# Performance work log

Hardware: AMD Instinct MI355X
Metric: run time of the kernel (lower is better)

The kernel has to match this reference:

```python
import jax, jax.numpy as jnp
import numpy as np

WIDTH = 1.0  # radial_width
AMPLITUDE = (WIDTH ** 0.5) * 1.772637204826652  # ~sqrt(pi*width)
BN_EPS = 1e-3  # keras BatchNormalization default


def sine_pos_encoding(seq_len, hidden, dtype):
    # keras_nlp.layers.SinePositionEncoding, max_wavelength=10000
    position = jnp.arange(seq_len, dtype=dtype)
    min_freq = jnp.asarray(1.0 / 10000.0, dtype)
    timescales = min_freq ** (2 * (jnp.arange(hidden) // 2).astype(dtype) / hidden)
    angles = position[:, None] * timescales[None, :]  # [T, H]
    odd = (jnp.arange(hidden) % 2).astype(dtype)
    return jnp.sin(angles) * (1 - odd) + jnp.cos(angles) * odd


def setup_inputs() -> dict:
    key = jax.random.key(0)
    ks = jax.random.split(key, 4)
    B, T, C, F, K, L = 16, 4096, 8, 64, 11, 4096
    x = jax.random.normal(ks[0], (B, T, C), jnp.float32)
    conv_w = jax.random.normal(ks[1], (K, C, F), jnp.float32) * 0.1
    conv_b = jnp.zeros((F,), jnp.float32)
    gamma = jnp.ones((F,), jnp.float32)
    beta = jnp.zeros((F,), jnp.float32)
    mean = jnp.zeros((F,), jnp.float32)
    var = jnp.ones((F,), jnp.float32)
    # HeNormal init for dense
    dense_w = jax.random.normal(ks[2], (F, L), jnp.float32) * (2.0 / F) ** 0.5
    dense_b = jnp.zeros((L,), jnp.float32)
    return dict(x=x, conv_w=conv_w, conv_b=conv_b, gamma=gamma, beta=beta,
                mean=mean, var=var, dense_w=dense_w, dense_b=dense_b)


def reference(x, conv_w, conv_b, gamma, beta, mean, var, dense_w, dense_b):
    B, T, C = x.shape
    F = conv_w.shape[-1]
    L = dense_w.shape[-1]
    # Conv1D same padding -> [B, T, F]
    h = jax.lax.conv_general_dilated(x, conv_w, (1,), 'SAME',
                                     dimension_numbers=('NWC', 'WIO', 'NWC')) + conv_b
    # BatchNorm (inference form)
    h = (h - mean) / jnp.sqrt(var + BN_EPS) * gamma + beta
    # Softmax over time axis
    h = jax.nn.softmax(h, axis=1)
    # sine positional encoding added
    h = h + sine_pos_encoding(T, F, x.dtype)
    # Dense with sigmoid, rescale to [-1, 1]
    d = jax.nn.sigmoid(h @ dense_w + dense_b) * 2.0 - 1.0  # [B, T, L]
    # ReductionLayer: sum over time -> shift weights [B, L]
    shift = jnp.sum(d, axis=1)
    # ShiftingLayer: Gaussian RBF warp matrix then matmul
    idx_in = jnp.arange(1, T + 1, dtype=x.dtype)                       # [T]
    scale = jnp.asarray(T / L, x.dtype)
    idx_sh = (jnp.arange(1, L + 1, dtype=x.dtype) + shift) * scale     # [B, L]
    M = idx_in[None, None, :] - idx_sh[:, :, None]                     # [B, L, T]
    M = jnp.exp(-(M * M) / WIDTH) / AMPLITUDE
    return jnp.matmul(M, x)  # [B, L, C]
```

## Files before the change

### kernel.cpp

```cpp
#include <hip/hip_runtime.h>
#include <stdint.h>

#define BB 16
#define TT 4096
#define CC 8
#define FF 64
#define KW 11
#define LL 4096

typedef __attribute__((ext_vector_type(8))) short short8;
typedef __attribute__((ext_vector_type(16))) float floatx16;

__device__ __forceinline__ unsigned short f2b(float f) {
    union { float f; uint32_t i; } v; v.f = f;
    uint32_t x = v.i;
    return (unsigned short)((x + 0x7fffu + ((x >> 16) & 1u)) >> 16);
}
__device__ __forceinline__ float b2f(unsigned short u) {
    union { uint32_t i; float f; } v; v.i = ((uint32_t)u) << 16; return v.f;
}

__global__ __launch_bounds__(256) void k_split(
        const float* __restrict__ dw, unsigned short* __restrict__ Wt) {
    const int idx  = blockIdx.x * 256 + threadIdx.x;
    const int j    = idx & 7;
    const int ln   = (idx >> 3) & 31;
    const int half = (idx >> 8) & 1;
    const int kf   = (idx >> 9) & 3;
    const int lt   = idx >> 11;
    const int l = lt * 32 + ln;
    const int k = kf * 16 + half * 8 + j;
    const float v = dw[(size_t)k * LL + l];
    const unsigned short hi = f2b(v);
    const unsigned short lo = f2b(v - b2f(hi));
    Wt[idx] = hi;
    Wt[262144 + idx] = lo;
}

__global__ __launch_bounds__(256) void k_sumexp(
        const float* __restrict__ x, const float* __restrict__ cw,
        const float* __restrict__ cb, const float* __restrict__ gm,
        const float* __restrict__ bt, const float* __restrict__ mn,
        const float* __restrict__ vr, float* __restrict__ sumexp) {
    __shared__ __align__(16) float xsm[(64 + KW - 1) * CC];
    __shared__ float red[4 * FF];
    const int tid = threadIdx.x;
    const int b  = blockIdx.x / (TT / 64);
    const int t0 = (blockIdx.x % (TT / 64)) * 64;
    const int f = tid & 63, ts = tid >> 6;

    float wreg[KW * CC];
#pragma unroll
    for (int kc = 0; kc < KW * CC; ++kc) wreg[kc] = cw[kc * FF + f];

    for (int i = tid; i < (64 + KW - 1) * CC; i += 256) {
        int row = i >> 3, c = i & 7;
        int t = t0 - (KW / 2) + row;
        xsm[i] = (t >= 0 && t < TT) ? x[((size_t)b * TT + t) * CC + c] : 0.0f;
    }
    const float s  = gm[f] * rsqrtf(vr[f] + 1e-3f);
    const float bb = bt[f] + (cb[f] - mn[f]) * s;
    __syncthreads();

    const float4* xv = (const float4*)xsm;
    float esum = 0.f;
#pragma unroll 2
    for (int i = 0; i < 16; ++i) {
        const int tt = ts + 4 * i;
        float acc = 0.f;
#pragma unroll
        for (int k = 0; k < KW; ++k) {
            const float4 xa = xv[(tt + k) * 2];
            const float4 xb = xv[(tt + k) * 2 + 1];
            acc = fmaf(xa.x, wreg[k * 8 + 0], acc);
            acc = fmaf(xa.y, wreg[k * 8 + 1], acc);
            acc = fmaf(xa.z, wreg[k * 8 + 2], acc);
            acc = fmaf(xa.w, wreg[k * 8 + 3], acc);
            acc = fmaf(xb.x, wreg[k * 8 + 4], acc);
            acc = fmaf(xb.y, wreg[k * 8 + 5], acc);
            acc = fmaf(xb.z, wreg[k * 8 + 6], acc);
            acc = fmaf(xb.w, wreg[k * 8 + 7], acc);
        }
        esum += __expf(fmaf(acc, s, bb));
    }
    red[ts * FF + f] = esum;
    __syncthreads();
    if (ts == 0) {
        float tot = red[f] + red[FF + f] + red[2 * FF + f] + red[3 * FF + f];
        atomicAdd(&sumexp[b * FF + f], tot);
    }
}

__global__ __launch_bounds__(256) void k_main(
        const float* __restrict__ x,  const float* __restrict__ cw,
        const float* __restrict__ cb, const float* __restrict__ gm,
        const float* __restrict__ bt, const float* __restrict__ mn,
        const float* __restrict__ vr, const unsigned short* __restrict__ Wt,
        const float* __restrict__ db, const float* __restrict__ sumexp,
        float* __restrict__ shiftsum) {
    __shared__ __align__(16) unsigned short As[16384];
    __shared__ __align__(16) float xsm[(128 + KW - 1) * CC];

    const int tid = threadIdx.x;
    const int b  = blockIdx.y;
    const int t0 = blockIdx.x * 128;
    const int f = tid & 63, tq = tid >> 6;

    float wreg[KW * CC];
#pragma unroll
    for (int kc = 0; kc < KW * CC; ++kc) wreg[kc] = cw[kc * FF + f];

    for (int i = tid; i < (128 + KW - 1) * CC; i += 256) {
        int row = i >> 3, c = i & 7;
        int t = t0 - (KW / 2) + row;
        xsm[i] = (t >= 0 && t < TT) ? x[((size_t)b * TT + t) * CC + c] : 0.0f;
    }
    const float s   = gm[f] * rsqrtf(vr[f] + 1e-3f);
    const float bbv = bt[f] + (cb[f] - mn[f]) * s;
    const float inv_se = 1.0f / sumexp[b * FF + f];
    const float tsf = exp2f(-0.20762050586796017f * (float)(f & ~1));
    const int kfh = ((f >> 4) << 1) | ((f >> 3) & 1);
    const int jj  = f & 7;
    __syncthreads();

    const float4* xv = (const float4*)xsm;
#pragma unroll 2
    for (int i = 0; i < 32; ++i) {
        const int tt = tq + 4 * i;
        float acc = 0.f;
#pragma unroll
        for (int k = 0; k < KW; ++k) {
            const float4 xa = xv[(tt + k) * 2];
            const float4 xb = xv[(tt + k) * 2 + 1];
            acc = fmaf(xa.x, wreg[k * 8 + 0], acc);
            acc = fmaf(xa.y, wreg[k * 8 + 1], acc);
            acc = fmaf(xa.z, wreg[k * 8 + 2], acc);
            acc = fmaf(xa.w, wreg[k * 8 + 3], acc);
            acc = fmaf(xb.x, wreg[k * 8 + 4], acc);
            acc = fmaf(xb.y, wreg[k * 8 + 5], acc);
            acc = fmaf(xb.z, wreg[k * 8 + 6], acc);
            acc = fmaf(xb.w, wreg[k * 8 + 7], acc);
        }
        float e = __expf(fmaf(acc, s, bbv));
        float ang = (float)(t0 + tt) * tsf;
        float p = (f & 1) ? cosf(ang) : sinf(ang);
        float h = fmaf(e, inv_se, p);
        const unsigned short hi = f2b(h);
        const unsigned short lo = f2b(h - b2f(hi));
        const int off = ((tt >> 5) * 8 + kfh) * 256 + (tt & 31) * 8 + jj;
        As[off] = hi;
        As[8192 + off] = lo;
    }
    __syncthreads();

    const int lane = tid & 63;
    const int wv   = tid >> 6;
    const int half = lane >> 5;
    const int ln31 = lane & 31;
    const int vbase = (half << 9) | (ln31 << 4);
    const char* Ab = (const char*)As;
    const char* Wb = (const char*)Wt;

    short8 Ahi[16], Alo[16];
#pragma unroll
    for (int nt = 0; nt < 4; ++nt)
#pragma unroll
        for (int kf = 0; kf < 4; ++kf) {
            const int ao = (nt * 8 + kf * 2) << 9;
            Ahi[nt * 4 + kf] = *reinterpret_cast<const short8*>(Ab + ao + vbase);
            Alo[nt * 4 + kf] = *reinterpret_cast<const short8*>(Ab + 16384 + ao + vbase);
        }

#pragma unroll 1
    for (int lt = 0; lt < 32; ++lt) {
        const int ltile = lt * 4 + wv;
        const int lbase = ltile * 32;
        const char* wp = Wb + ((size_t)ltile << 12) + vbase;
        short8 Whi[4], Wlo[4];
#pragma unroll
        for (int kf = 0; kf < 4; ++kf) {
            Whi[kf] = *reinterpret_cast<const short8*>(wp + kf * 1024);
            Wlo[kf] = *reinterpret_cast<const short8*>(wp + 524288 + kf * 1024);
        }
        const float dbl = db[lbase + ln31];

        float ss[4] = {0.f, 0.f, 0.f, 0.f};
#pragma unroll
        for (int nt = 0; nt < 4; ++nt) {
            floatx16 acc = {0.f, 0.f, 0.f, 0.f, 0.f, 0.f, 0.f, 0.f,
                            0.f, 0.f, 0.f, 0.f, 0.f, 0.f, 0.f, 0.f};
#pragma unroll
            for (int kf = 0; kf < 4; ++kf) {
                acc = __builtin_amdgcn_mfma_f32_32x32x16_bf16(Ahi[nt * 4 + kf], Whi[kf], acc, 0, 0, 0);
                acc = __builtin_amdgcn_mfma_f32_32x32x16_bf16(Alo[nt * 4 + kf], Whi[kf], acc, 0, 0, 0);
                acc = __builtin_amdgcn_mfma_f32_32x32x16_bf16(Ahi[nt * 4 + kf], Wlo[kf], acc, 0, 0, 0);
            }
#pragma unroll
            for (int r = 0; r < 16; ++r) {
                float z = acc[r] + dbl;
                float e = __expf(-z);
                ss[r & 3] += __builtin_amdgcn_rcpf(1.0f + e);
            }
        }
        float ssum = (ss[0] + ss[1]) + (ss[2] + ss[3]);
        ssum += __shfl_xor(ssum, 32);
        if (half == 0)
            atomicAdd(shiftsum + (size_t)b * LL + lbase + ln31, ssum);
    }
}

__global__ __launch_bounds__(256) void k_warp(
        const float* __restrict__ shiftsum, const float* __restrict__ x,
        float* __restrict__ out) {
    const int idx = blockIdx.x * 256 + threadIdx.x;
    const int l = idx & (LL - 1);
    const int b = idx >> 12;
    const float sh = fmaf(2.0f, shiftsum[idx], -(float)TT);
    const float scale = (float)TT / (float)LL;
    const float center = ((float)(l + 1) + sh) * scale;
    const float R = 7.0f;
    int tlo = (int)ceilf(center - 1.0f - R);
    int thi = (int)floorf(center - 1.0f + R);
    if (tlo < 0) tlo = 0;
    if (thi > TT - 1) thi = TT - 1;
    float acc[CC];
#pragma unroll
    for (int c = 0; c < CC; ++c) acc[c] = 0.f;
    const float inv_amp = (float)(1.0 / 1.772637204826652);
    for (int t = tlo; t <= thi; ++t) {
        float d = (float)(t + 1) - center;
        float w = __expf(-d * d) * inv_amp;
        const float4 x0 = *reinterpret_cast<const float4*>(x + ((size_t)b * TT + t) * CC);
        const float4 x1 = *reinterpret_cast<const float4*>(x + ((size_t)b * TT + t) * CC + 4);
        acc[0] = fmaf(w, x0.x, acc[0]);
        acc[1] = fmaf(w, x0.y, acc[1]);
        acc[2] = fmaf(w, x0.z, acc[2]);
        acc[3] = fmaf(w, x0.w, acc[3]);
        acc[4] = fmaf(w, x1.x, acc[4]);
        acc[5] = fmaf(w, x1.y, acc[5]);
        acc[6] = fmaf(w, x1.z, acc[6]);
        acc[7] = fmaf(w, x1.w, acc[7]);
    }
    float* o = out + (size_t)idx * CC;
    *reinterpret_cast<float4*>(o)     = make_float4(acc[0], acc[1], acc[2], acc[3]);
    *reinterpret_cast<float4*>(o + 4) = make_float4(acc[4], acc[5], acc[6], acc[7]);
}

extern "C" void kernel_launch(void* const* d_in, const int* in_sizes, int n_in,
                              void* d_out, int out_size, void* d_ws, size_t ws_size,
                              hipStream_t stream) {
    const float* x  = (const float*)d_in[0];
    const float* cw = (const float*)d_in[1];
    const float* cb = (const float*)d_in[2];
    const float* gm = (const float*)d_in[3];
    const float* bt = (const float*)d_in[4];
    const float* mn = (const float*)d_in[5];
    const float* vr = (const float*)d_in[6];
    const float* dw = (const float*)d_in[7];
    const float* db = (const float*)d_in[8];

    float* sumexp      = (float*)d_ws;
    float* shiftsum    = sumexp + BB * FF;
    unsigned short* Wt = (unsigned short*)(shiftsum + BB * LL);

    hipMemsetAsync(sumexp, 0, (size_t)(BB * FF + BB * LL) * sizeof(float), stream);

    k_split<<<(FF * LL) / 256, 256, 0, stream>>>(dw, Wt);
    k_sumexp<<<BB * (TT / 64), 256, 0, stream>>>(x, cw, cb, gm, bt, mn, vr, sumexp);
    k_main<<<dim3(TT / 128, BB), 256, 0, stream>>>(x, cw, cb, gm, bt, mn, vr,
                                                   Wt, db, sumexp, shiftsum);
    k_warp<<<(BB * LL) / 256, 256, 0, stream>>>(shiftsum, x, (float*)d_out);
}
```

Before: 219.9 us.

## Raise k_main to 512 threads, stream A from LDS, cheapen exp/sin/sigmoid math

k_main now runs 8 waves per block. Each wave handles half as many conv rows and L-tiles as before. A-fragments are reloaded from LDS inside the MFMA loop instead of being kept in 32 registers, which cuts register pressure so the tighter launch bounds can allow more resident waves. Per-row sin/cos calls are replaced by a rotation recurrence, and __expf is replaced by exp2 with pre-scaled constants. In the sigmoid reduction, four reciprocals are merged into one. Risks: 512,4 launch bounds may force spills of the 88-float conv weights, and the merged reciprocal can overflow for large exponents.

```diff
diff --git a/kernel.cpp b/kernel.cpp
--- a/kernel.cpp
+++ b/kernel.cpp
@@ -7,6 +7,8 @@
 #define FF 64
 #define KW 11
 #define LL 4096
+
+#define L2E 1.442695040888963f
 
 typedef __attribute__((ext_vector_type(8))) short short8;
 typedef __attribute__((ext_vector_type(16))) float floatx16;
@@ -60,6 +62,7 @@
     }
     const float s  = gm[f] * rsqrtf(vr[f] + 1e-3f);
     const float bb = bt[f] + (cb[f] - mn[f]) * s;
+    const float s2 = s * L2E, b2 = bb * L2E;
     __syncthreads();
 
     const float4* xv = (const float4*)xsm;
@@ -81,7 +84,7 @@
             acc = fmaf(xb.z, wreg[k * 8 + 6], acc);
             acc = fmaf(xb.w, wreg[k * 8 + 7], acc);
         }
-        esum += __expf(fmaf(acc, s, bb));
+        esum += __builtin_amdgcn_exp2f(fmaf(acc, s2, b2));
     }
     red[ts * FF + f] = esum;
     __syncthreads();
@@ -91,7 +94,7 @@
     }
 }
 
-__global__ __launch_bounds__(256) void k_main(
+__global__ __launch_bounds__(512, 4) void k_main(
         const float* __restrict__ x,  const float* __restrict__ cw,
         const float* __restrict__ cb, const float* __restrict__ gm,
         const float* __restrict__ bt, const float* __restrict__ mn,
@@ -110,23 +113,28 @@
 #pragma unroll
     for (int kc = 0; kc < KW * CC; ++kc) wreg[kc] = cw[kc * FF + f];
 
-    for (int i = tid; i < (128 + KW - 1) * CC; i += 256) {
+    for (int i = tid; i < (128 + KW - 1) * CC; i += 512) {
         int row = i >> 3, c = i & 7;
         int t = t0 - (KW / 2) + row;
         xsm[i] = (t >= 0 && t < TT) ? x[((size_t)b * TT + t) * CC + c] : 0.0f;
     }
     const float s   = gm[f] * rsqrtf(vr[f] + 1e-3f);
     const float bbv = bt[f] + (cb[f] - mn[f]) * s;
+    const float s2 = s * L2E, b2 = bbv * L2E;
     const float inv_se = 1.0f / sumexp[b * FF + f];
     const float tsf = exp2f(-0.20762050586796017f * (float)(f & ~1));
     const int kfh = ((f >> 4) << 1) | ((f >> 3) & 1);
     const int jj  = f & 7;
+    const float ang0 = (float)(t0 + tq) * tsf;
+    const float dA = 8.0f * tsf;
+    float sv = sinf(ang0), cv = cosf(ang0);
+    const float sd = sinf(dA), cd = cosf(dA);
     __syncthreads();
 
     const float4* xv = (const float4*)xsm;
 #pragma unroll 2
-    for (int i = 0; i < 32; ++i) {
-        const int tt = tq + 4 * i;
+    for (int i = 0; i < 16; ++i) {
+        const int tt = tq + 8 * i;
         float acc = 0.f;
 #pragma unroll
         for (int k = 0; k < KW; ++k) {
@@ -141,15 +149,17 @@
             acc = fmaf(xb.z, wreg[k * 8 + 6], acc);
             acc = fmaf(xb.w, wreg[k * 8 + 7], acc);
         }
-        float e = __expf(fmaf(acc, s, bbv));
-        float ang = (float)(t0 + tt) * tsf;
-        float p = (f & 1) ? cosf(ang) : sinf(ang);
+        float e = __builtin_amdgcn_exp2f(fmaf(acc, s2, b2));
+        float p = (f & 1) ? cv : sv;
         float h = fmaf(e, inv_se, p);
         const unsigned short hi = f2b(h);
         const unsigned short lo = f2b(h - b2f(hi));
         const int off = ((tt >> 5) * 8 + kfh) * 256 + (tt & 31) * 8 + jj;
         As[off] = hi;
         As[8192 + off] = lo;
+        float ns = fmaf(sv, cd, cv * sd);
+        float nc = fmaf(cv, cd, -(sv * sd));
+        sv = ns; cv = nc;
     }
     __syncthreads();
 
@@ -161,19 +171,9 @@
     const char* Ab = (const char*)As;
     const char* Wb = (const char*)Wt;
 
-    short8 Ahi[16], Alo[16];
-#pragma unroll
-    for (int nt = 0; nt < 4; ++nt)
-#pragma unroll
-        for (int kf = 0; kf < 4; ++kf) {
-            const int ao = (nt * 8 + kf * 2) << 9;
-            Ahi[nt * 4 + kf] = *reinterpret_cast<const short8*>(Ab + ao + vbase);
-            Alo[nt * 4 + kf] = *reinterpret_cast<const short8*>(Ab + 16384 + ao + vbase);
-        }
-
 #pragma unroll 1
-    for (int lt = 0; lt < 32; ++lt) {
-        const int ltile = lt * 4 + wv;
+    for (int lt = 0; lt < 16; ++lt) {
+        const int ltile = lt * 8 + wv;
         const int lbase = ltile * 32;
         const char* wp = Wb + ((size_t)ltile << 12) + vbase;
         short8 Whi[4], Wlo[4];
@@ -182,7 +182,7 @@
             Whi[kf] = *reinterpret_cast<const short8*>(wp + kf * 1024);
             Wlo[kf] = *reinterpret_cast<const short8*>(wp + 524288 + kf * 1024);
         }
-        const float dbl = db[lbase + ln31];
+        const float dbn = db[lbase + ln31] * (-L2E);
 
         float ss[4] = {0.f, 0.f, 0.f, 0.f};
 #pragma unroll
@@ -191,15 +191,23 @@
                             0.f, 0.f, 0.f, 0.f, 0.f, 0.f, 0.f, 0.f};
 #pragma unroll
             for (int kf = 0; kf < 4; ++kf) {
-                acc = __builtin_amdgcn_mfma_f32_32x32x16_bf16(Ahi[nt * 4 + kf], Whi[kf], acc, 0, 0, 0);
-                acc = __builtin_amdgcn_mfma_f32_32x32x16_bf16(Alo[nt * 4 + kf], Whi[kf], acc, 0, 0, 0);
-                acc = __builtin_amdgcn_mfma_f32_32x32x16_bf16(Ahi[nt * 4 + kf], Wlo[kf], acc, 0, 0, 0);
+                const int ao = (nt * 8 + kf * 2) << 9;
+                short8 Ahi = *reinterpret_cast<const short8*>(Ab + ao + vbase);
+                short8 Alo = *reinterpret_cast<const short8*>(Ab + 16384 + ao + vbase);
+                acc = __builtin_amdgcn_mfma_f32_32x32x16_bf16(Ahi, Whi[kf], acc, 0, 0, 0);
+                acc = __builtin_amdgcn_mfma_f32_32x32x16_bf16(Alo, Whi[kf], acc, 0, 0, 0);
+                acc = __builtin_amdgcn_mfma_f32_32x32x16_bf16(Ahi, Wlo[kf], acc, 0, 0, 0);
             }
 #pragma unroll
-            for (int r = 0; r < 16; ++r) {
-                float z = acc[r] + dbl;
-                float e = __expf(-z);
-                ss[r & 3] += __builtin_amdgcn_rcpf(1.0f + e);
+            for (int q = 0; q < 4; ++q) {
+                float e0 = __builtin_amdgcn_exp2f(fmaf(acc[4 * q + 0], -L2E, dbn));
+                float e1 = __builtin_amdgcn_exp2f(fmaf(acc[4 * q + 1], -L2E, dbn));
+                float e2 = __builtin_amdgcn_exp2f(fmaf(acc[4 * q + 2], -L2E, dbn));
+                float e3 = __builtin_amdgcn_exp2f(fmaf(acc[4 * q + 3], -L2E, dbn));
+                float a0 = 1.f + e0, a1 = 1.f + e1, a2 = 1.f + e2, a3 = 1.f + e3;
+                float p01 = a0 * a1, p23 = a2 * a3;
+                float num = fmaf(a0 + a1, p23, (a2 + a3) * p01);
+                ss[q] = fmaf(num, __builtin_amdgcn_rcpf(p01 * p23), ss[q]);
             }
         }
         float ssum = (ss[0] + ss[1]) + (ss[2] + ss[3]);
@@ -267,7 +275,7 @@
 
     k_split<<<(FF * LL) / 256, 256, 0, stream>>>(dw, Wt);
     k_sumexp<<<BB * (TT / 64), 256, 0, stream>>>(x, cw, cb, gm, bt, mn, vr, sumexp);
-    k_main<<<dim3(TT / 128, BB), 256, 0, stream>>>(x, cw, cb, gm, bt, mn, vr,
+    k_main<<<dim3(TT / 128, BB), 512, 0, stream>>>(x, cw, cb, gm, bt, mn, vr,
                                                    Wt, db, sumexp, shiftsum);
     k_warp<<<(BB * LL) / 256, 256, 0, stream>>>(shiftsum, x, (float*)d_out);
 }
```

Result: slower. 284.8 us (+29.5%).
